# Optimization experiments

Hardware: AMD Instinct MI355X
Metric: run time of the kernel (lower is better)

Reference implementation:

```python
import jax, jax.numpy as jnp
import numpy as np
from jax import lax

B, L, LQ, D_IN, ET, H, INIT_EMBED = 16, 256, 64, 32, 128, 4, 8
DIM = 2 * D_IN          # attention value/feature dim (x concat mask)
ETK = ET // H           # per-head time-embedding dim


def _lin(key, fan_in, shape):
    b = 1.0 / np.sqrt(fan_in)
    return jax.random.uniform(key, shape, jnp.float32, -b, b)


def setup_inputs() -> dict:
    key = jax.random.key(0)
    ks = jax.random.split(key, 24)
    inp = {
        "x": jax.random.normal(ks[0], (B, L, D_IN), jnp.float32),
        "time_steps": jnp.sort(jax.random.uniform(ks[1], (B, L), jnp.float32), axis=-1),
        "mask": (jax.random.uniform(ks[2], (B, L, D_IN)) > 0.5).astype(jnp.float32),
        "query": jnp.linspace(0.0, 1.0, LQ, dtype=jnp.float32),
        # time embedding: Linear(1,1) and Linear(1, ET-1)
        "w_lin": _lin(ks[3], 1, (1,)), "b_lin": _lin(ks[4], 1, (1,)),
        "w_per": _lin(ks[5], 1, (ET - 1,)), "b_per": _lin(ks[6], 1, (ET - 1,)),
        # attention projections (stored as (in,out))
        "Wq": _lin(ks[7], ET, (ET, ET)), "bq": _lin(ks[8], ET, (ET,)),
        "Wk": _lin(ks[9], ET, (ET, ET)), "bk": _lin(ks[10], ET, (ET,)),
        "Wo": _lin(ks[11], H * DIM, (H * DIM, ET)), "bo": _lin(ks[12], H * DIM, (ET,)),
        # vanilla RNN (tanh)
        "W_ih": _lin(ks[13], ET, (ET, ET)), "b_ih": _lin(ks[14], ET, (ET,)),
        "W_hh": _lin(ks[15], ET, (ET, ET)), "b_hh": _lin(ks[16], ET, (ET,)),
        "r1_w": _lin(ks[17], ET, (ET, 128)), "r1_b": _lin(ks[17], ET, (128,)),
        "r2_w": _lin(ks[18], 128, (128, 128)), "r2_b": _lin(ks[18], 128, (128,)),
        "r3_w": _lin(ks[19], 128, (128, ET)), "r3_b": _lin(ks[19], 128, (ET,)),
        "r4_w": _lin(ks[20], ET, (ET, INIT_EMBED)), "r4_b": _lin(ks[20], ET, (INIT_EMBED,)),
    }
    return inp


def reference(x, time_steps, mask, query,
              w_lin, b_lin, w_per, b_per,
              Wq, bq, Wk, bk, Wo, bo,
              W_ih, b_ih, W_hh, b_hh,
              r1_w, r1_b, r2_w, r2_b, r3_w, r3_b, r4_w, r4_b):
    def time_embed(tt):  # (...,) -> (..., ET)
        tt = tt[..., None]
        return jnp.concatenate([tt * w_lin + b_lin,
                                jnp.sin(tt * w_per + b_per)], axis=-1)

    xc = jnp.concatenate([x, mask], axis=-1)          # (B,L,DIM) value
    m2 = jnp.concatenate([mask, mask], axis=-1)       # (B,L,DIM)

    kemb = time_embed(time_steps)                     # (B,L,ET)
    qemb = time_embed(query)                          # (LQ,ET)

    q = (qemb @ Wq + bq).reshape(LQ, H, ETK).transpose(1, 0, 2)       # (H,LQ,ETK)
    k = (kemb @ Wk + bk).reshape(B, L, H, ETK).transpose(0, 2, 1, 3)  # (B,H,L,ETK)

    scores = jnp.einsum('hqe,bhke->bhqk', q, k) / np.sqrt(ETK)        # (B,H,LQ,L)
    # per-feature mask broadcast: (B,H,LQ,L,DIM)
    s5 = jnp.where(m2[:, None, None, :, :] == 0, -1e9, scores[..., None])
    p = jax.nn.softmax(s5, axis=-2)                   # softmax over keys L
    att = jnp.einsum('bhqkd,bkd->bhqd', p, xc)        # (B,H,LQ,DIM)
    att = att.transpose(0, 2, 1, 3).reshape(B, LQ, H * DIM)
    out = att @ Wo + bo                               # (B,LQ,ET)

    # vanilla tanh RNN, return final hidden state
    def step(h, xt):
        h = jnp.tanh(xt @ W_ih + b_ih + h @ W_hh + b_hh)
        return h, None
    h0 = jnp.zeros((B, ET), out.dtype)
    hT, _ = lax.scan(step, h0, out.transpose(1, 0, 2))  # scan over LQ

    y = hT @ r1_w + r1_b
    y = y @ r2_w + r2_b
    y = y @ r3_w + r3_b
    y = y @ r4_w + r4_b                               # (B, INIT_EMBED)
    return y
```

## Files before the change

kernel.cpp:

```cpp
#include <hip/hip_runtime.h>
#include <hip/hip_bf16.h>


#define NB 16
#define NL 256
#define NLQ 64
#define NDIN 32
#define NET 128
#define NH 4
#define NETK 32

#define HPAD 136
#define PAD(i) ((i) + 4 * ((i) >> 6))

__global__ __launch_bounds__(128) void k_embed_proj(
    const float* __restrict__ ts, const float* __restrict__ query,
    const float* __restrict__ w_lin, const float* __restrict__ b_lin,
    const float* __restrict__ w_per, const float* __restrict__ b_per,
    const float* __restrict__ Wk, const float* __restrict__ bk,
    const float* __restrict__ Wq, const float* __restrict__ bq,
    float* __restrict__ kproj, float* __restrict__ qproj) {
  __shared__ float emb[8 * NET];
  int g = blockIdx.x;
  int j = threadIdx.x;
  bool isQ = (g >= 512);
  int base = (isQ ? g - 512 : g) * 8;
  float wl_ = w_lin[0], bl_ = b_lin[0];
  float wp = (j > 0) ? w_per[j - 1] : 0.f;
  float bp = (j > 0) ? b_per[j - 1] : 0.f;
#pragma unroll
  for (int rr = 0; rr < 8; rr++) {
    float t = isQ ? query[base + rr] : ts[base + rr];
    emb[rr * NET + j] = (j == 0) ? (t * wl_ + bl_) : sinf(t * wp + bp);
  }
  __syncthreads();
  const float* W = isQ ? Wq : Wk;
  float bias = isQ ? bq[j] : bk[j];
  float acc[8];
#pragma unroll
  for (int rr = 0; rr < 8; rr++) acc[rr] = bias;
#pragma unroll 4
  for (int i = 0; i < NET; i++) {
    float wv = W[i * NET + j];
#pragma unroll
    for (int rr = 0; rr < 8; rr++) acc[rr] += emb[rr * NET + i] * wv;
  }
  float* dst = isQ ? qproj : kproj;
#pragma unroll
  for (int rr = 0; rr < 8; rr++) dst[(size_t)(base + rr) * NET + j] = acc[rr];
}

__global__ __launch_bounds__(256) void k_attn(
    const float* __restrict__ x, const float* __restrict__ mask,
    const float* __restrict__ qproj, const float* __restrict__ kproj,
    float* __restrict__ att) {
  const float SC = 0.17677669529663687f;
  int blk = blockIdx.x;
  int qg = blk & 15;
  int h  = (blk >> 4) & 3;
  int b  = blk >> 6;
  int t  = threadIdx.x;

  __shared__ float xs[NL * NDIN];
  __shared__ unsigned mb[NL];
  __shared__ float es[4 * NL];
  __shared__ float qs[4 * NETK];

  if (t < 128) {
    int qq = t >> 5, i = t & 31;
    qs[t] = qproj[(qg * 4 + qq) * NET + h * NETK + i];
  }
  {
    const float4* src = (const float4*)(x + (size_t)b * NL * NDIN);
    float4* dst = (float4*)xs;
#pragma unroll
    for (int u = 0; u < 8; u++) dst[t + 256 * u] = src[t + 256 * u];
  }
  {
    const float4* mr4 = (const float4*)(mask + (size_t)(b * NL + t) * NDIN);
    unsigned bits = 0;
#pragma unroll
    for (int u = 0; u < 8; u++) {
      float4 m = mr4[u];
      bits |= (m.x != 0.f ? 1u : 0u) << (4 * u);
      bits |= (m.y != 0.f ? 1u : 0u) << (4 * u + 1);
      bits |= (m.z != 0.f ? 1u : 0u) << (4 * u + 2);
      bits |= (m.w != 0.f ? 1u : 0u) << (4 * u + 3);
    }
    mb[t] = bits;
  }
  __syncthreads();

  {
    float kr[NETK];
    const float4* kp =
        (const float4*)(kproj + (size_t)(b * NL + t) * NET + h * NETK);
#pragma unroll
    for (int i = 0; i < 8; i++) {
      float4 v = kp[i];
      kr[4 * i] = v.x; kr[4 * i + 1] = v.y;
      kr[4 * i + 2] = v.z; kr[4 * i + 3] = v.w;
    }
#pragma unroll
    for (int qq = 0; qq < 4; qq++) {
      const float* qv = &qs[qq * NETK];
      float s0 = 0.f, s1 = 0.f;
#pragma unroll
      for (int i = 0; i < NETK; i += 2) {
        s0 += qv[i] * kr[i];
        s1 += qv[i + 1] * kr[i + 1];
      }
      es[qq * NL + t] = __expf((s0 + s1) * SC);
    }
  }
  __syncthreads();

  {
    int s = t & 1;
    int p = t >> 1;
    int qq = p >> 5;
    int c  = p & 31;
    int k0 = s * 128;
    float den = 0.f, num = 0.f, sumx = 0.f;
#pragma unroll 4
    for (int k = k0; k < k0 + 128; k++) {
      float e  = es[qq * NL + k];
      float mv = ((mb[k] >> c) & 1u) ? 1.f : 0.f;
      float xv = xs[k * NDIN + c];
      sumx += xv;
      e *= mv;
      den += e;
      num += e * xv;
    }
    den  += __shfl_xor(den, 1, 64);
    num  += __shfl_xor(num, 1, 64);
    sumx += __shfl_xor(sumx, 1, 64);
    if (s == 0) {
      bool any = (den > 0.f);
      float ax = any ? (num / den) : (sumx * (1.f / 256.f));
      float am = any ? 1.f : 0.f;
      int q = qg * 4 + qq;
      float* ao = att + (size_t)((b * NLQ + q) * NH + h) * 64;
      ao[c]      = ax;
      ao[32 + c] = am;
    }
  }
}

__global__ __launch_bounds__(128) void k_out_xw(
    const float* __restrict__ att,
    const float* __restrict__ Wo, const float* __restrict__ bo,
    const float* __restrict__ Wih, const float* __restrict__ bih,
    const float* __restrict__ bhh, float* __restrict__ XW) {
  int r = blockIdx.x;
  int j = threadIdx.x;
  __shared__ float arow[NH * 64];
  __shared__ float orow[NET];
  arow[j]       = att[(size_t)r * 256 + j];
  arow[j + 128] = att[(size_t)r * 256 + 128 + j];
  __syncthreads();
  float a0 = bo[j], a1 = 0.f, a2 = 0.f, a3 = 0.f;
#pragma unroll 8
  for (int u = 0; u < 256; u += 4) {
    a0 += arow[u]     * Wo[(u)     * NET + j];
    a1 += arow[u + 1] * Wo[(u + 1) * NET + j];
    a2 += arow[u + 2] * Wo[(u + 2) * NET + j];
    a3 += arow[u + 3] * Wo[(u + 3) * NET + j];
  }
  orow[j] = (a0 + a1) + (a2 + a3);
  __syncthreads();
  float b0 = bih[j] + bhh[j], b1 = 0.f, b2 = 0.f, b3 = 0.f;
#pragma unroll 8
  for (int e = 0; e < NET; e += 4) {
    b0 += orow[e]     * Wih[(e)     * NET + j];
    b1 += orow[e + 1] * Wih[(e + 1) * NET + j];
    b2 += orow[e + 2] * Wih[(e + 2) * NET + j];
    b3 += orow[e + 3] * Wih[(e + 3) * NET + j];
  }
  XW[(size_t)r * NET + j] = (b0 + b1) + (b2 + b3);
}

__device__ __forceinline__ void layer128(const float* src_lds,
                                         const float* __restrict__ W,
                                         const float* __restrict__ bvec,
                                         float* dst_lds, int j, int s) {
  const float4* h4 = (const float4*)(src_lds + s * 68);
  float a0 = 0.f, a1 = 0.f, a2 = 0.f, a3 = 0.f;
#pragma unroll
  for (int i = 0; i < 16; i++) {
    float4 hv = h4[i];
    int base = (s * 64 + 4 * i) * NET + j;
    a0 += hv.x * W[base];
    a1 += hv.y * W[base + NET];
    a2 += hv.z * W[base + 2 * NET];
    a3 += hv.w * W[base + 3 * NET];
  }
  float acc = (a0 + a1) + (a2 + a3);
  acc += __shfl_xor(acc, 1, 64);
  if (s == 0) dst_lds[PAD(j)] = acc + bvec[j];
}

__global__ __launch_bounds__(256, 1) void k_rnn(
    const float* __restrict__ XW, const float* __restrict__ Whh,
    const float* __restrict__ r1w, const float* __restrict__ r1b,
    const float* __restrict__ r2w, const float* __restrict__ r2b,
    const float* __restrict__ r3w, const float* __restrict__ r3b,
    const float* __restrict__ r4w, const float* __restrict__ r4b,
    float* __restrict__ out) {
  int b = blockIdx.x;
  int tid = threadIdx.x;
  int s = tid & 1;
  int j = tid >> 1;
  __shared__ float xwl[NLQ * NET];
  __shared__ float hb[2][HPAD];
  __shared__ float tmp[HPAD];

  {
    const float4* src = (const float4*)(XW + (size_t)b * NLQ * NET);
    float4* dst = (float4*)xwl;
#pragma unroll
    for (int u = 0; u < 8; u++) dst[tid + 256 * u] = src[tid + 256 * u];
  }
  float w[64];
#pragma unroll
  for (int i = 0; i < 64; i++) w[i] = Whh[(s * 64 + i) * NET + j];

  if (tid < 128) hb[0][PAD(tid)] = 0.f;
  __syncthreads();

  for (int t = 0; t < NLQ; t++) {
    float xwv = xwl[t * NET + j];
    const float4* h4 = (const float4*)&hb[t & 1][s * 68];
    float a0 = 0.f, a1 = 0.f, a2 = 0.f, a3 = 0.f;
#pragma unroll
    for (int i = 0; i < 16; i++) {
      float4 hv = h4[i];
      a0 += hv.x * w[4 * i];
      a1 += hv.y * w[4 * i + 1];
      a2 += hv.z * w[4 * i + 2];
      a3 += hv.w * w[4 * i + 3];
    }
    float acc = (a0 + a1) + (a2 + a3);
    acc += __shfl_xor(acc, 1, 64);
    if (s == 0) {
      float z = acc + xwv;
      float e2 = __expf(2.f * z);
      hb[(t + 1) & 1][PAD(j)] = 1.f - 2.f / (e2 + 1.f);
    }
    __syncthreads();
  }

  layer128(hb[0], r1w, r1b, tmp, j, s);
  __syncthreads();
  layer128(tmp, r2w, r2b, hb[1], j, s);
  __syncthreads();
  layer128(hb[1], r3w, r3b, hb[0], j, s);
  __syncthreads();
  if (tid < 64) {
    int jj = tid >> 3, p = tid & 7;
    float y = 0.f;
#pragma unroll
    for (int i = 0; i < 16; i++) {
      int ii = p * 16 + i;
      y += hb[0][PAD(ii)] * r4w[ii * 8 + jj];
    }
    y += __shfl_xor(y, 1, 64);
    y += __shfl_xor(y, 2, 64);
    y += __shfl_xor(y, 4, 64);
    if (p == 0) out[b * 8 + jj] = y + r4b[jj];
  }
}

extern "C" void kernel_launch(void* const* d_in, const int* in_sizes, int n_in,
                              void* d_out, int out_size, void* d_ws, size_t ws_size,
                              hipStream_t stream) {
  const float* x     = (const float*)d_in[0];
  const float* ts    = (const float*)d_in[1];
  const float* mask  = (const float*)d_in[2];
  const float* query = (const float*)d_in[3];
  const float* w_lin = (const float*)d_in[4];
  const float* b_lin = (const float*)d_in[5];
  const float* w_per = (const float*)d_in[6];
  const float* b_per = (const float*)d_in[7];
  const float* Wq    = (const float*)d_in[8];
  const float* bq    = (const float*)d_in[9];
  const float* Wk    = (const float*)d_in[10];
  const float* bk    = (const float*)d_in[11];
  const float* Wo    = (const float*)d_in[12];
  const float* bo    = (const float*)d_in[13];
  const float* Wih   = (const float*)d_in[14];
  const float* bih   = (const float*)d_in[15];
  const float* Whh   = (const float*)d_in[16];
  const float* bhh   = (const float*)d_in[17];
  const float* r1w   = (const float*)d_in[18];
  const float* r1b   = (const float*)d_in[19];
  const float* r2w   = (const float*)d_in[20];
  const float* r2b   = (const float*)d_in[21];
  const float* r3w   = (const float*)d_in[22];
  const float* r3b   = (const float*)d_in[23];
  const float* r4w   = (const float*)d_in[24];
  const float* r4b   = (const float*)d_in[25];
  float* out = (float*)d_out;

  float* ws    = (float*)d_ws;
  float* kproj = ws;
  float* qproj = ws + 524288;
  float* att   = ws + 532480;
  float* XW    = ws + 794624;

  k_embed_proj<<<520, 128, 0, stream>>>(
      ts, query, w_lin, b_lin, w_per, b_per, Wk, bk, Wq, bq, kproj, qproj);
  k_attn<<<NB * NH * 16, 256, 0, stream>>>(x, mask, qproj, kproj, att);
  k_out_xw<<<NB * NLQ, 128, 0, stream>>>(att, Wo, bo, Wih, bih, bhh, XW);
  k_rnn<<<NB, 256, 0, stream>>>(XW, Whh, r1w, r1b, r2w, r2b, r3w, r3b,
                                r4w, r4b, out);
}
```

Baseline: 186.0 us.

## Fuse attention with output and input projections, process all heads per block

Merges the attention kernel and the Wo/W_ih projection kernel into one, so each block handles all four heads for a batch and query group, then computes the output and RNN input projections from LDS. This removes one launch and the att round-trip through global memory, and shares x/mask loads across heads. The cost is a 4x smaller grid (256 blocks), more LDS per block, and more serial work per block, which may lower occupancy and parallelism.

```diff
diff --git a/kernel.cpp b/kernel.cpp
--- a/kernel.cpp
+++ b/kernel.cpp
@@ -12,6 +12,9 @@
 
 #define HPAD 136
 #define PAD(i) ((i) + 4 * ((i) >> 6))
+
+#define ESS 20
+#define ORP 132
 
 __global__ __launch_bounds__(128) void k_embed_proj(
     const float* __restrict__ ts, const float* __restrict__ query,
@@ -50,25 +53,30 @@
   for (int rr = 0; rr < 8; rr++) dst[(size_t)(base + rr) * NET + j] = acc[rr];
 }
 
-__global__ __launch_bounds__(256) void k_attn(
+__global__ __launch_bounds__(256) void k_attn_fused(
     const float* __restrict__ x, const float* __restrict__ mask,
     const float* __restrict__ qproj, const float* __restrict__ kproj,
-    float* __restrict__ att) {
+    const float* __restrict__ Wo, const float* __restrict__ bo,
+    const float* __restrict__ Wih, const float* __restrict__ bih,
+    const float* __restrict__ bhh, float* __restrict__ XW) {
   const float SC = 0.17677669529663687f;
   int blk = blockIdx.x;
   int qg = blk & 15;
-  int h  = (blk >> 4) & 3;
-  int b  = blk >> 6;
+  int b  = blk >> 4;
   int t  = threadIdx.x;
 
   __shared__ float xs[NL * NDIN];
   __shared__ unsigned mb[NL];
-  __shared__ float es[4 * NL];
-  __shared__ float qs[4 * NETK];
-
-  if (t < 128) {
-    int qq = t >> 5, i = t & 31;
-    qs[t] = qproj[(qg * 4 + qq) * NET + h * NETK + i];
+  __shared__ float es[NL * ESS];
+  __shared__ float qs[4 * NET];
+  __shared__ float arow[4 * 256];
+  __shared__ float orow[4 * ORP];
+
+  {
+    int qq = t >> 7;
+    int e  = t & 127;
+    qs[qq * NET + e]       = qproj[(size_t)(qg * 4 + qq) * NET + e];
+    qs[(qq + 2) * NET + e] = qproj[(size_t)(qg * 4 + qq + 2) * NET + e];
   }
   {
     const float4* src = (const float4*)(x + (size_t)b * NL * NDIN);
@@ -91,7 +99,7 @@
   }
   __syncthreads();
 
-  {
+  for (int h = 0; h < NH; h++) {
     float kr[NETK];
     const float4* kp =
         (const float4*)(kproj + (size_t)(b * NL + t) * NET + h * NETK);
@@ -103,14 +111,14 @@
     }
 #pragma unroll
     for (int qq = 0; qq < 4; qq++) {
-      const float* qv = &qs[qq * NETK];
+      const float* qv = &qs[qq * NET + h * NETK];
       float s0 = 0.f, s1 = 0.f;
 #pragma unroll
       for (int i = 0; i < NETK; i += 2) {
         s0 += qv[i] * kr[i];
         s1 += qv[i + 1] * kr[i + 1];
       }
-      es[qq * NL + t] = __expf((s0 + s1) * SC);
+      es[t * ESS + qq * 4 + h] = __expf((s0 + s1) * SC);
     }
   }
   __syncthreads();
@@ -121,63 +129,68 @@
     int qq = p >> 5;
     int c  = p & 31;
     int k0 = s * 128;
-    float den = 0.f, num = 0.f, sumx = 0.f;
+    float den[NH] = {0.f, 0.f, 0.f, 0.f};
+    float num[NH] = {0.f, 0.f, 0.f, 0.f};
+    float sumx = 0.f;
 #pragma unroll 4
     for (int k = k0; k < k0 + 128; k++) {
-      float e  = es[qq * NL + k];
+      float xv = xs[k * NDIN + c];
       float mv = ((mb[k] >> c) & 1u) ? 1.f : 0.f;
-      float xv = xs[k * NDIN + c];
+      float4 e4 = *(const float4*)(es + k * ESS + qq * 4);
       sumx += xv;
-      e *= mv;
-      den += e;
-      num += e * xv;
-    }
-    den  += __shfl_xor(den, 1, 64);
-    num  += __shfl_xor(num, 1, 64);
+      float e0 = e4.x * mv, e1 = e4.y * mv, e2 = e4.z * mv, e3 = e4.w * mv;
+      den[0] += e0; num[0] += e0 * xv;
+      den[1] += e1; num[1] += e1 * xv;
+      den[2] += e2; num[2] += e2 * xv;
+      den[3] += e3; num[3] += e3 * xv;
+    }
     sumx += __shfl_xor(sumx, 1, 64);
+#pragma unroll
+    for (int h = 0; h < NH; h++) {
+      den[h] += __shfl_xor(den[h], 1, 64);
+      num[h] += __shfl_xor(num[h], 1, 64);
+    }
     if (s == 0) {
-      bool any = (den > 0.f);
-      float ax = any ? (num / den) : (sumx * (1.f / 256.f));
-      float am = any ? 1.f : 0.f;
-      int q = qg * 4 + qq;
-      float* ao = att + (size_t)((b * NLQ + q) * NH + h) * 64;
-      ao[c]      = ax;
-      ao[32 + c] = am;
-    }
-  }
-}
-
-__global__ __launch_bounds__(128) void k_out_xw(
-    const float* __restrict__ att,
-    const float* __restrict__ Wo, const float* __restrict__ bo,
-    const float* __restrict__ Wih, const float* __restrict__ bih,
-    const float* __restrict__ bhh, float* __restrict__ XW) {
-  int r = blockIdx.x;
-  int j = threadIdx.x;
-  __shared__ float arow[NH * 64];
-  __shared__ float orow[NET];
-  arow[j]       = att[(size_t)r * 256 + j];
-  arow[j + 128] = att[(size_t)r * 256 + 128 + j];
-  __syncthreads();
-  float a0 = bo[j], a1 = 0.f, a2 = 0.f, a3 = 0.f;
-#pragma unroll 8
-  for (int u = 0; u < 256; u += 4) {
-    a0 += arow[u]     * Wo[(u)     * NET + j];
-    a1 += arow[u + 1] * Wo[(u + 1) * NET + j];
-    a2 += arow[u + 2] * Wo[(u + 2) * NET + j];
-    a3 += arow[u + 3] * Wo[(u + 3) * NET + j];
-  }
-  orow[j] = (a0 + a1) + (a2 + a3);
-  __syncthreads();
-  float b0 = bih[j] + bhh[j], b1 = 0.f, b2 = 0.f, b3 = 0.f;
-#pragma unroll 8
-  for (int e = 0; e < NET; e += 4) {
-    b0 += orow[e]     * Wih[(e)     * NET + j];
-    b1 += orow[e + 1] * Wih[(e + 1) * NET + j];
-    b2 += orow[e + 2] * Wih[(e + 2) * NET + j];
-    b3 += orow[e + 3] * Wih[(e + 3) * NET + j];
-  }
-  XW[(size_t)r * NET + j] = (b0 + b1) + (b2 + b3);
+      float meanx = sumx * (1.f / 256.f);
+#pragma unroll
+      for (int h = 0; h < NH; h++) {
+        bool any = (den[h] > 0.f);
+        arow[qq * 256 + h * 64 + c]      = any ? (num[h] / den[h]) : meanx;
+        arow[qq * 256 + h * 64 + 32 + c] = any ? 1.f : 0.f;
+      }
+    }
+  }
+  __syncthreads();
+
+  {
+    int j = t & 127;
+    int half = t >> 7;
+    float o0 = bo[j], o1 = o0;
+#pragma unroll 4
+    for (int u = 0; u < 256; u++) {
+      float w = Wo[(size_t)u * NET + j];
+      o0 += arow[half * 256 + u] * w;
+      o1 += arow[(half + 2) * 256 + u] * w;
+    }
+    orow[half * ORP + j] = o0;
+    orow[(half + 2) * ORP + j] = o1;
+  }
+  __syncthreads();
+
+  {
+    int j = t & 127;
+    int half = t >> 7;
+    float a0 = bih[j] + bhh[j], a1 = a0;
+#pragma unroll 4
+    for (int e = 0; e < NET; e++) {
+      float w = Wih[(size_t)e * NET + j];
+      a0 += orow[half * ORP + e] * w;
+      a1 += orow[(half + 2) * ORP + e] * w;
+    }
+    int q0 = qg * 4 + half;
+    XW[(size_t)(b * NLQ + q0) * NET + j]     = a0;
+    XW[(size_t)(b * NLQ + q0 + 2) * NET + j] = a1;
+  }
 }
 
 __device__ __forceinline__ void layer128(const float* src_lds,
@@ -305,13 +318,12 @@
   float* ws    = (float*)d_ws;
   float* kproj = ws;
   float* qproj = ws + 524288;
-  float* att   = ws + 532480;
-  float* XW    = ws + 794624;
+  float* XW    = ws + 532480;
 
   k_embed_proj<<<520, 128, 0, stream>>>(
       ts, query, w_lin, b_lin, w_per, b_per, Wk, bk, Wq, bq, kproj, qproj);
-  k_attn<<<NB * NH * 16, 256, 0, stream>>>(x, mask, qproj, kproj, att);
-  k_out_xw<<<NB * NLQ, 128, 0, stream>>>(att, Wo, bo, Wih, bih, bhh, XW);
+  k_attn_fused<<<NB * 16, 256, 0, stream>>>(
+      x, mask, qproj, kproj, Wo, bo, Wih, bih, bhh, XW);
   k_rnn<<<NB, 256, 0, stream>>>(XW, Whh, r1w, r1b, r2w, r2b, r3w, r3b,
                                 r4w, r4b, out);
 }
```

Measured after the change: 195.2 us. 5.0% more time.

## Precompute mask bitmasks once and restructure attention reduction across key slices

Applied to the files above, without the earlier changes.

Mask bit-packing moves from every attention block into 16 extra blocks of the embed/projection kernel, which write a global bitmask buffer. The attention kernel no longer stages x and the mask in LDS. Instead each thread handles all four queries for one feature over a 32-key slice and reads x directly from global/L2, with partial sums combined by a cross-wave shuffle and LDS reduction. The projection and Wo/Wih loops also switch to float4 LDS reads. This cuts the redundant mask conversion and the large LDS staging per block, at the cost of more uncached-looking global reads of x and an extra reduction step.

```diff
diff --git a/kernel.cpp b/kernel.cpp
--- a/kernel.cpp
+++ b/kernel.cpp
@@ -15,14 +15,37 @@
 
 __global__ __launch_bounds__(128) void k_embed_proj(
     const float* __restrict__ ts, const float* __restrict__ query,
+    const float* __restrict__ mask,
     const float* __restrict__ w_lin, const float* __restrict__ b_lin,
     const float* __restrict__ w_per, const float* __restrict__ b_per,
     const float* __restrict__ Wk, const float* __restrict__ bk,
     const float* __restrict__ Wq, const float* __restrict__ bq,
-    float* __restrict__ kproj, float* __restrict__ qproj) {
-  __shared__ float emb[8 * NET];
+    float* __restrict__ kproj, float* __restrict__ qproj,
+    unsigned* __restrict__ mbg) {
+  __shared__ __align__(16) float emb[8 * NET];
   int g = blockIdx.x;
   int j = threadIdx.x;
+
+  if (g >= 520) {
+    int b = g - 520;
+#pragma unroll
+    for (int half = 0; half < 2; half++) {
+      int r = j + 128 * half;
+      const float4* mr4 = (const float4*)(mask + (size_t)(b * NL + r) * NDIN);
+      unsigned bits = 0;
+#pragma unroll
+      for (int u = 0; u < 8; u++) {
+        float4 m = mr4[u];
+        bits |= (m.x != 0.f ? 1u : 0u) << (4 * u);
+        bits |= (m.y != 0.f ? 1u : 0u) << (4 * u + 1);
+        bits |= (m.z != 0.f ? 1u : 0u) << (4 * u + 2);
+        bits |= (m.w != 0.f ? 1u : 0u) << (4 * u + 3);
+      }
+      mbg[b * NL + r] = bits;
+    }
+    return;
+  }
+
   bool isQ = (g >= 512);
   int base = (isQ ? g - 512 : g) * 8;
   float wl_ = w_lin[0], bl_ = b_lin[0];
@@ -39,11 +62,17 @@
   float acc[8];
 #pragma unroll
   for (int rr = 0; rr < 8; rr++) acc[rr] = bias;
-#pragma unroll 4
-  for (int i = 0; i < NET; i++) {
-    float wv = W[i * NET + j];
-#pragma unroll
-    for (int rr = 0; rr < 8; rr++) acc[rr] += emb[rr * NET + i] * wv;
+#pragma unroll 2
+  for (int i = 0; i < NET; i += 4) {
+    float w0 = W[(size_t)i * NET + j];
+    float w1 = W[(size_t)(i + 1) * NET + j];
+    float w2 = W[(size_t)(i + 2) * NET + j];
+    float w3 = W[(size_t)(i + 3) * NET + j];
+#pragma unroll
+    for (int rr = 0; rr < 8; rr++) {
+      float4 e4 = *(const float4*)&emb[rr * NET + i];
+      acc[rr] += e4.x * w0 + e4.y * w1 + e4.z * w2 + e4.w * w3;
+    }
   }
   float* dst = isQ ? qproj : kproj;
 #pragma unroll
@@ -51,7 +80,7 @@
 }
 
 __global__ __launch_bounds__(256) void k_attn(
-    const float* __restrict__ x, const float* __restrict__ mask,
+    const float* __restrict__ x, const unsigned* __restrict__ mbg,
     const float* __restrict__ qproj, const float* __restrict__ kproj,
     float* __restrict__ att) {
   const float SC = 0.17677669529663687f;
@@ -61,88 +90,91 @@
   int b  = blk >> 6;
   int t  = threadIdx.x;
 
-  __shared__ float xs[NL * NDIN];
-  __shared__ unsigned mb[NL];
-  __shared__ float es[4 * NL];
-  __shared__ float qs[4 * NETK];
-
-  if (t < 128) {
-    int qq = t >> 5, i = t & 31;
-    qs[t] = qproj[(qg * 4 + qq) * NET + h * NETK + i];
-  }
+  __shared__ __align__(16) float es4[NL * 4];
+  __shared__ float part[3 * 32 * 9];
+
   {
-    const float4* src = (const float4*)(x + (size_t)b * NL * NDIN);
-    float4* dst = (float4*)xs;
-#pragma unroll
-    for (int u = 0; u < 8; u++) dst[t + 256 * u] = src[t + 256 * u];
-  }
-  {
-    const float4* mr4 = (const float4*)(mask + (size_t)(b * NL + t) * NDIN);
-    unsigned bits = 0;
-#pragma unroll
-    for (int u = 0; u < 8; u++) {
-      float4 m = mr4[u];
-      bits |= (m.x != 0.f ? 1u : 0u) << (4 * u);
-      bits |= (m.y != 0.f ? 1u : 0u) << (4 * u + 1);
-      bits |= (m.z != 0.f ? 1u : 0u) << (4 * u + 2);
-      bits |= (m.w != 0.f ? 1u : 0u) << (4 * u + 3);
-    }
-    mb[t] = bits;
-  }
-  __syncthreads();
-
-  {
+    int k = t;
     float kr[NETK];
     const float4* kp =
-        (const float4*)(kproj + (size_t)(b * NL + t) * NET + h * NETK);
+        (const float4*)(kproj + (size_t)(b * NL + k) * NET + h * NETK);
 #pragma unroll
     for (int i = 0; i < 8; i++) {
       float4 v = kp[i];
       kr[4 * i] = v.x; kr[4 * i + 1] = v.y;
       kr[4 * i + 2] = v.z; kr[4 * i + 3] = v.w;
     }
+    float ev[4];
 #pragma unroll
     for (int qq = 0; qq < 4; qq++) {
-      const float* qv = &qs[qq * NETK];
+      const float* qv = qproj + (size_t)(qg * 4 + qq) * NET + h * NETK;
       float s0 = 0.f, s1 = 0.f;
 #pragma unroll
       for (int i = 0; i < NETK; i += 2) {
         s0 += qv[i] * kr[i];
         s1 += qv[i + 1] * kr[i + 1];
       }
-      es[qq * NL + t] = __expf((s0 + s1) * SC);
-    }
-  }
-  __syncthreads();
-
+      ev[qq] = __expf((s0 + s1) * SC);
+    }
+    *(float4*)&es4[k * 4] = make_float4(ev[0], ev[1], ev[2], ev[3]);
+  }
+  __syncthreads();
+
+  int kq = t >> 5, c = t & 31;
+  float den[4] = {0.f, 0.f, 0.f, 0.f};
+  float num[4] = {0.f, 0.f, 0.f, 0.f};
+  float sumx = 0.f;
   {
-    int s = t & 1;
-    int p = t >> 1;
-    int qq = p >> 5;
-    int c  = p & 31;
-    int k0 = s * 128;
-    float den = 0.f, num = 0.f, sumx = 0.f;
+    const float* xb = x + (size_t)b * NL * NDIN;
+    const unsigned* mbb = mbg + b * NL;
+    int k0 = kq * 32;
 #pragma unroll 4
-    for (int k = k0; k < k0 + 128; k++) {
-      float e  = es[qq * NL + k];
-      float mv = ((mb[k] >> c) & 1u) ? 1.f : 0.f;
-      float xv = xs[k * NDIN + c];
+    for (int kk = 0; kk < 32; kk++) {
+      int k = k0 + kk;
+      float4 e4 = *(const float4*)&es4[k * 4];
+      float xv = xb[(size_t)k * NDIN + c];
+      float mv = ((mbb[k] >> c) & 1u) ? 1.f : 0.f;
       sumx += xv;
-      e *= mv;
-      den += e;
-      num += e * xv;
-    }
-    den  += __shfl_xor(den, 1, 64);
-    num  += __shfl_xor(num, 1, 64);
-    sumx += __shfl_xor(sumx, 1, 64);
-    if (s == 0) {
-      bool any = (den > 0.f);
-      float ax = any ? (num / den) : (sumx * (1.f / 256.f));
-      float am = any ? 1.f : 0.f;
-      int q = qg * 4 + qq;
-      float* ao = att + (size_t)((b * NLQ + q) * NH + h) * 64;
-      ao[c]      = ax;
-      ao[32 + c] = am;
+      float e0 = e4.x * mv, e1 = e4.y * mv, e2 = e4.z * mv, e3 = e4.w * mv;
+      den[0] += e0; num[0] += e0 * xv;
+      den[1] += e1; num[1] += e1 * xv;
+      den[2] += e2; num[2] += e2 * xv;
+      den[3] += e3; num[3] += e3 * xv;
+    }
+  }
+  sumx += __shfl_xor(sumx, 32, 64);
+#pragma unroll
+  for (int q = 0; q < 4; q++) {
+    den[q] += __shfl_xor(den[q], 32, 64);
+    num[q] += __shfl_xor(num[q], 32, 64);
+  }
+  {
+    int w = t >> 6, lane = t & 63;
+    if (w > 0 && lane < 32) {
+      float* p = &part[((w - 1) * 32 + c) * 9];
+#pragma unroll
+      for (int q = 0; q < 4; q++) { p[q] = den[q]; p[4 + q] = num[q]; }
+      p[8] = sumx;
+    }
+  }
+  __syncthreads();
+
+  if (t < 32) {
+#pragma unroll
+    for (int ww = 0; ww < 3; ww++) {
+      const float* p = &part[(ww * 32 + t) * 9];
+#pragma unroll
+      for (int q = 0; q < 4; q++) { den[q] += p[q]; num[q] += p[4 + q]; }
+      sumx += p[8];
+    }
+    float meanx = sumx * (1.f / 256.f);
+#pragma unroll
+    for (int qq = 0; qq < 4; qq++) {
+      bool any = (den[qq] > 0.f);
+      float* ao =
+          att + (size_t)(((b * NLQ + qg * 4 + qq) * NH) + h) * 64;
+      ao[t]      = any ? (num[qq] / den[qq]) : meanx;
+      ao[32 + t] = any ? 1.f : 0.f;
     }
   }
 }
@@ -154,28 +186,30 @@
     const float* __restrict__ bhh, float* __restrict__ XW) {
   int r = blockIdx.x;
   int j = threadIdx.x;
-  __shared__ float arow[NH * 64];
-  __shared__ float orow[NET];
+  __shared__ __align__(16) float arow[NH * 64];
+  __shared__ __align__(16) float orow[NET];
   arow[j]       = att[(size_t)r * 256 + j];
   arow[j + 128] = att[(size_t)r * 256 + 128 + j];
   __syncthreads();
   float a0 = bo[j], a1 = 0.f, a2 = 0.f, a3 = 0.f;
-#pragma unroll 8
+#pragma unroll 4
   for (int u = 0; u < 256; u += 4) {
-    a0 += arow[u]     * Wo[(u)     * NET + j];
-    a1 += arow[u + 1] * Wo[(u + 1) * NET + j];
-    a2 += arow[u + 2] * Wo[(u + 2) * NET + j];
-    a3 += arow[u + 3] * Wo[(u + 3) * NET + j];
+    float4 av = *(const float4*)&arow[u];
+    a0 += av.x * Wo[(size_t)u * NET + j];
+    a1 += av.y * Wo[(size_t)(u + 1) * NET + j];
+    a2 += av.z * Wo[(size_t)(u + 2) * NET + j];
+    a3 += av.w * Wo[(size_t)(u + 3) * NET + j];
   }
   orow[j] = (a0 + a1) + (a2 + a3);
   __syncthreads();
   float b0 = bih[j] + bhh[j], b1 = 0.f, b2 = 0.f, b3 = 0.f;
-#pragma unroll 8
+#pragma unroll 4
   for (int e = 0; e < NET; e += 4) {
-    b0 += orow[e]     * Wih[(e)     * NET + j];
-    b1 += orow[e + 1] * Wih[(e + 1) * NET + j];
-    b2 += orow[e + 2] * Wih[(e + 2) * NET + j];
-    b3 += orow[e + 3] * Wih[(e + 3) * NET + j];
+    float4 ov = *(const float4*)&orow[e];
+    b0 += ov.x * Wih[(size_t)e * NET + j];
+    b1 += ov.y * Wih[(size_t)(e + 1) * NET + j];
+    b2 += ov.z * Wih[(size_t)(e + 2) * NET + j];
+    b3 += ov.w * Wih[(size_t)(e + 3) * NET + j];
   }
   XW[(size_t)r * NET + j] = (b0 + b1) + (b2 + b3);
 }
@@ -307,10 +341,12 @@
   float* qproj = ws + 524288;
   float* att   = ws + 532480;
   float* XW    = ws + 794624;
-
-  k_embed_proj<<<520, 128, 0, stream>>>(
-      ts, query, w_lin, b_lin, w_per, b_per, Wk, bk, Wq, bq, kproj, qproj);
-  k_attn<<<NB * NH * 16, 256, 0, stream>>>(x, mask, qproj, kproj, att);
+  unsigned* mbg = (unsigned*)(ws + 925696);
+
+  k_embed_proj<<<536, 128, 0, stream>>>(
+      ts, query, mask, w_lin, b_lin, w_per, b_per, Wk, bk, Wq, bq,
+      kproj, qproj, mbg);
+  k_attn<<<NB * NH * 16, 256, 0, stream>>>(x, mbg, qproj, kproj, att);
   k_out_xw<<<NB * NLQ, 128, 0, stream>>>(att, Wo, bo, Wih, bih, bhh, XW);
   k_rnn<<<NB, 256, 0, stream>>>(XW, Whh, r1w, r1b, r2w, r2b, r3w, r3b,
                                 r4w, r4b, out);
```

New measurement: 178.9 us. -3.8%, faster.
